# Performance work log

Hardware: AMD Instinct MI355X
Metric: run time of the kernel (lower is better)

The kernel has to match this reference:

```python
import jax, jax.numpy as jnp
import numpy as np

WEIGHT_THRESH = 0.5
EPS = 1e-5
B, N = 4096, 1024


def setup_inputs() -> dict:
    key = jax.random.key(0)
    k1, k2, k3 = jax.random.split(key, 3)
    src = jax.random.normal(k1, (B, N, 3), dtype=jnp.float32)
    tgt = jax.random.normal(k2, (B, N, 3), dtype=jnp.float32)
    w = jax.random.uniform(k3, (B, N), dtype=jnp.float32)
    return {"src_points": src, "tgt_points": tgt, "weights": w}


def _weighted_procrustes(src, ref, w):
    # threshold + normalize weights
    w = jnp.where(w < WEIGHT_THRESH, jnp.zeros_like(w), w)
    w = w / (jnp.sum(w, axis=1, keepdims=True) + EPS)
    w = w[:, :, None]                       # (B, N, 1)
    # weighted centroids
    src_c = jnp.sum(src * w, axis=1, keepdims=True)   # (B, 1, 3)
    ref_c = jnp.sum(ref * w, axis=1, keepdims=True)   # (B, 1, 3)
    src0 = src - src_c
    ref0 = ref - ref_c
    # weighted cross-covariance H = src0^T @ (w * ref0): (B, 3, 3)
    H = jnp.einsum('bni,bnj->bij', src0, w * ref0)
    U, S, Vh = jnp.linalg.svd(H)            # torch.svd returns V, jnp returns Vh
    V = jnp.swapaxes(Vh, 1, 2)
    Ut = jnp.swapaxes(U, 1, 2)
    det = jnp.linalg.det(V @ Ut)            # (B,)
    sgn = jnp.sign(det)
    # D = diag(1, 1, sign(det)); V @ D scales the last column of V
    D = jnp.stack([jnp.ones_like(sgn), jnp.ones_like(sgn), sgn], axis=-1)  # (B, 3)
    R = (V * D[:, None, :]) @ Ut            # (B, 3, 3)
    # t = ref_c - R @ src_c
    t = (jnp.swapaxes(ref_c, 1, 2) - R @ jnp.swapaxes(src_c, 1, 2))[:, :, 0]  # (B, 3)
    return R, t


def reference(src_points, tgt_points, weights):
    return _weighted_procrustes(src_points, tgt_points, weights)
```

## Files before the change

### kernel.cpp

```cpp
#include <hip/hip_runtime.h>
#include <math.h>

#define WTHRESH 0.5f
#define EPSV    1e-5f

__device__ __forceinline__ void gload_lds16(const float4* g, float4* l) {
  __builtin_amdgcn_global_load_lds(
      (const __attribute__((address_space(1))) void*)g,
      (__attribute__((address_space(3))) void*)l, 16, 0, 0);
}

template <int CTRL>
__device__ __forceinline__ float dpp_add(float x) {
  int xi = __builtin_bit_cast(int, x);
  int mv = __builtin_amdgcn_update_dpp(0, xi, CTRL, 0xF, 0xF, true);
  return x + __builtin_bit_cast(float, mv);
}

#define JROT(app,aqq,apq, arp,arq, vAp,vAq, vBp,vBq, vCp,vCq)                 \
  do {                                                                        \
    float _apq = (apq);                                                       \
    if (fabsf(_apq) > 1e-30f) {                                               \
      float _tau = ((aqq) - (app)) * 0.5f / _apq;                             \
      float _t = copysignf(1.0f, _tau) / (fabsf(_tau) + sqrtf(1.0f + _tau*_tau)); \
      float _c = 1.0f / sqrtf(1.0f + _t*_t);                                  \
      float _s = _t * _c;                                                     \
      float _app = (app), _aqq = (aqq);                                       \
      (app) = _app - _t * _apq;                                               \
      (aqq) = _aqq + _t * _apq;                                               \
      (apq) = 0.0f;                                                           \
      float _arp = (arp), _arq = (arq);                                       \
      (arp) = _c * _arp - _s * _arq;                                          \
      (arq) = _s * _arp + _c * _arq;                                          \
      { float _vp=(vAp), _vq=(vAq); (vAp)=_c*_vp-_s*_vq; (vAq)=_s*_vp+_c*_vq; } \
      { float _vp=(vBp), _vq=(vBq); (vBp)=_c*_vp-_s*_vq; (vBq)=_s*_vp+_c*_vq; } \
      { float _vp=(vCp), _vq=(vCq); (vCp)=_c*_vp-_s*_vq; (vCq)=_s*_vp+_c*_vq; } \
    }                                                                         \
  } while (0)

#define CSWAP(li,lj, x0,x1, y0,y1, z0,z1)                                     \
  do { if ((li) < (lj)) {                                                     \
    float _t;                                                                 \
    _t=(li); (li)=(lj); (lj)=_t;                                              \
    _t=(x0); (x0)=(x1); (x1)=_t;                                              \
    _t=(y0); (y0)=(y1); (y1)=_t;                                              \
    _t=(z0); (z0)=(z1); (z1)=_t;                                              \
  } } while (0)

__global__ __launch_bounds__(256) void wproc_reduce(
    const float* __restrict__ src, const float* __restrict__ tgt,
    const float* __restrict__ wts, float* __restrict__ ws)
{
  __shared__ float4 lds[1792];

  const int b    = blockIdx.x;
  const int tid  = threadIdx.x;
  const int wave = tid >> 6;
  const int lane = tid & 63;

  const float4* sg = reinterpret_cast<const float4*>(src + (size_t)b * 3072);
  const float4* tg = reinterpret_cast<const float4*>(tgt + (size_t)b * 3072);
  const float4* wg = reinterpret_cast<const float4*>(wts + (size_t)b * 1024);

  #pragma unroll
  for (int i = 0; i < 3; ++i) {
    const int c = wave * 192 + i * 64;
    gload_lds16(sg + c + lane, &lds[c]);
  }
  #pragma unroll
  for (int i = 0; i < 3; ++i) {
    const int c = wave * 192 + i * 64;
    gload_lds16(tg + c + lane, &lds[768 + c]);
  }
  {
    const int c = wave * 64;
    gload_lds16(wg + c + lane, &lds[1536 + c]);
  }
  __syncthreads();

  float4 sA = lds[3*tid+0], sB = lds[3*tid+1], sC = lds[3*tid+2];
  float4 tA = lds[768 + 3*tid+0], tB = lds[768 + 3*tid+1], tC = lds[768 + 3*tid+2];
  float4 wv = lds[1536 + tid];

  float acc[16];
  #pragma unroll
  for (int k = 0; k < 16; ++k) acc[k] = 0.0f;

  float PX[4][3] = {{sA.x,sA.y,sA.z},{sA.w,sB.x,sB.y},{sB.z,sB.w,sC.x},{sC.y,sC.z,sC.w}};
  float PY[4][3] = {{tA.x,tA.y,tA.z},{tA.w,tB.x,tB.y},{tB.z,tB.w,tC.x},{tC.y,tC.z,tC.w}};
  float WW[4]    = {wv.x, wv.y, wv.z, wv.w};

  #pragma unroll
  for (int k = 0; k < 4; ++k) {
    float w  = (WW[k] < WTHRESH) ? 0.0f : WW[k];
    float x0 = PX[k][0], x1 = PX[k][1], x2 = PX[k][2];
    float y0 = PY[k][0], y1 = PY[k][1], y2 = PY[k][2];
    acc[0] += w;
    acc[1] += w*x0; acc[2] += w*x1; acc[3] += w*x2;
    acc[4] += w*y0; acc[5] += w*y1; acc[6] += w*y2;
    float wx0 = w*x0, wx1 = w*x1, wx2 = w*x2;
    acc[7]  += wx0*y0; acc[8]  += wx0*y1; acc[9]  += wx0*y2;
    acc[10] += wx1*y0; acc[11] += wx1*y1; acc[12] += wx1*y2;
    acc[13] += wx2*y0; acc[14] += wx2*y1; acc[15] += wx2*y2;
  }

  #pragma unroll
  for (int k = 0; k < 16; ++k) acc[k] = dpp_add<0x111>(acc[k]);
  #pragma unroll
  for (int k = 0; k < 16; ++k) acc[k] = dpp_add<0x112>(acc[k]);
  #pragma unroll
  for (int k = 0; k < 16; ++k) acc[k] = dpp_add<0x114>(acc[k]);
  #pragma unroll
  for (int k = 0; k < 16; ++k) acc[k] = dpp_add<0x118>(acc[k]);
  #pragma unroll
  for (int k = 0; k < 16; ++k) acc[k] = dpp_add<0x142>(acc[k]);
  #pragma unroll
  for (int k = 0; k < 16; ++k) acc[k] = dpp_add<0x143>(acc[k]);

  if (lane == 63) {
    float* o = ws + ((size_t)b * 4 + wave) * 16;
    #pragma unroll
    for (int k = 0; k < 16; ++k) o[k] = acc[k];
  }
}

__global__ __launch_bounds__(256) void wproc_svd(
    const float* __restrict__ ws, float* __restrict__ outR,
    float* __restrict__ outT, int B)
{
  const int b = blockIdx.x * 256 + threadIdx.x;
  if (b >= B) return;

  const float4* p4 = reinterpret_cast<const float4*>(ws + (size_t)b * 64);
  float4 F4[4];
  #pragma unroll
  for (int j = 0; j < 4; ++j) {
    float4 a = p4[j], bb = p4[j+4], c = p4[j+8], d = p4[j+12];
    F4[j].x = a.x + bb.x + c.x + d.x;
    F4[j].y = a.y + bb.y + c.y + d.y;
    F4[j].z = a.z + bb.z + c.z + d.z;
    F4[j].w = a.w + bb.w + c.w + d.w;
  }
  float f[16] = {F4[0].x,F4[0].y,F4[0].z,F4[0].w, F4[1].x,F4[1].y,F4[1].z,F4[1].w,
                 F4[2].x,F4[2].y,F4[2].z,F4[2].w, F4[3].x,F4[3].y,F4[3].z,F4[3].w};

  const float inv  = 1.0f / (f[0] + EPSV);
  const float cx0 = f[1]*inv, cx1 = f[2]*inv, cx2 = f[3]*inv;
  const float cy0 = f[4]*inv, cy1 = f[5]*inv, cy2 = f[6]*inv;
  const float ssum = f[0] * inv;
  const float g = 2.0f - ssum;

  float H00 = f[7]*inv  - g*cx0*cy0, H01 = f[8]*inv  - g*cx0*cy1, H02 = f[9]*inv  - g*cx0*cy2;
  float H10 = f[10]*inv - g*cx1*cy0, H11 = f[11]*inv - g*cx1*cy1, H12 = f[12]*inv - g*cx1*cy2;
  float H20 = f[13]*inv - g*cx2*cy0, H21 = f[14]*inv - g*cx2*cy1, H22 = f[15]*inv - g*cx2*cy2;

  float a00 = H00*H00 + H10*H10 + H20*H20;
  float a11 = H01*H01 + H11*H11 + H21*H21;
  float a22 = H02*H02 + H12*H12 + H22*H22;
  float a01 = H00*H01 + H10*H11 + H20*H21;
  float a02 = H00*H02 + H10*H12 + H20*H22;
  float a12 = H01*H02 + H11*H12 + H21*H22;

  float v00=1.f,v01=0.f,v02=0.f, v10=0.f,v11=1.f,v12=0.f, v20=0.f,v21=0.f,v22=1.f;

  #pragma unroll
  for (int sweep = 0; sweep < 8; ++sweep) {
    JROT(a00,a11,a01, a02,a12, v00,v01, v10,v11, v20,v21);
    JROT(a00,a22,a02, a01,a12, v00,v02, v10,v12, v20,v22);
    JROT(a11,a22,a12, a01,a02, v01,v02, v11,v12, v21,v22);
  }

  CSWAP(a00,a11, v00,v01, v10,v11, v20,v21);
  CSWAP(a00,a22, v00,v02, v10,v12, v20,v22);
  CSWAP(a11,a22, v01,v02, v11,v12, v21,v22);

  float u00 = H00*v00 + H01*v10 + H02*v20;
  float u10 = H10*v00 + H11*v10 + H12*v20;
  float u20 = H20*v00 + H21*v10 + H22*v20;
  float u01 = H00*v01 + H01*v11 + H02*v21;
  float u11 = H10*v01 + H11*v11 + H12*v21;
  float u21 = H20*v01 + H21*v11 + H22*v21;
  float u02 = H00*v02 + H01*v12 + H02*v22;
  float u12 = H10*v02 + H11*v12 + H12*v22;
  float u22 = H20*v02 + H21*v12 + H22*v22;

  float n0 = sqrtf(u00*u00 + u10*u10 + u20*u20);
  float n1 = sqrtf(u01*u01 + u11*u11 + u21*u21);
  float n2 = sqrtf(u02*u02 + u12*u12 + u22*u22);

  float R00,R01,R02,R10,R11,R12,R20,R21,R22;

  if (n0 < 1e-20f) {
    R00=1.f;R01=0.f;R02=0.f; R10=0.f;R11=1.f;R12=0.f; R20=0.f;R21=0.f;R22=1.f;
  } else {
    float i0 = 1.0f / n0;
    u00*=i0; u10*=i0; u20*=i0;

    if (n1 > 1e-7f * n0) {
      float i1 = 1.0f / n1;
      u01*=i1; u11*=i1; u21*=i1;
    } else {
      float ax = fabsf(u00), ay = fabsf(u10), az = fabsf(u20);
      float e0,e1,e2;
      if (ax <= ay && ax <= az)      { e0=1.f; e1=0.f; e2=0.f; }
      else if (ay <= az)             { e0=0.f; e1=1.f; e2=0.f; }
      else                           { e0=0.f; e1=0.f; e2=1.f; }
      u01 = u10*e2 - u20*e1;
      u11 = u20*e0 - u00*e2;
      u21 = u00*e1 - u10*e0;
      float nn = 1.0f / sqrtf(u01*u01 + u11*u11 + u21*u21);
      u01*=nn; u11*=nn; u21*=nn;
    }

    if (n2 > 1e-7f * n0) {
      float i2 = 1.0f / n2;
      u02*=i2; u12*=i2; u22*=i2;
    } else {
      u02 = u10*u21 - u20*u11;
      u12 = u20*u01 - u00*u21;
      u22 = u00*u11 - u10*u01;
    }

    float detU = u00*(u11*u22 - u12*u21) - u01*(u10*u22 - u12*u20) + u02*(u10*u21 - u11*u20);
    float detV = v00*(v11*v22 - v12*v21) - v01*(v10*v22 - v12*v20) + v02*(v10*v21 - v11*v20);
    float sgn = (detU * detV < 0.0f) ? -1.0f : 1.0f;

    R00 = v00*u00 + v01*u01 + sgn*v02*u02;
    R01 = v00*u10 + v01*u11 + sgn*v02*u12;
    R02 = v00*u20 + v01*u21 + sgn*v02*u22;
    R10 = v10*u00 + v11*u01 + sgn*v12*u02;
    R11 = v10*u10 + v11*u11 + sgn*v12*u12;
    R12 = v10*u20 + v11*u21 + sgn*v12*u22;
    R20 = v20*u00 + v21*u01 + sgn*v22*u02;
    R21 = v20*u10 + v21*u11 + sgn*v22*u12;
    R22 = v20*u20 + v21*u21 + sgn*v22*u22;
  }

  float t0 = cy0 - (R00*cx0 + R01*cx1 + R02*cx2);
  float t1 = cy1 - (R10*cx0 + R11*cx1 + R12*cx2);
  float t2 = cy2 - (R20*cx0 + R21*cx1 + R22*cx2);

  float* Rb = outR + (size_t)b * 9;
  Rb[0]=R00; Rb[1]=R01; Rb[2]=R02;
  Rb[3]=R10; Rb[4]=R11; Rb[5]=R12;
  Rb[6]=R20; Rb[7]=R21; Rb[8]=R22;
  float* tb = outT + (size_t)b * 3;
  tb[0]=t0; tb[1]=t1; tb[2]=t2;
}

extern "C" void kernel_launch(void* const* d_in, const int* in_sizes, int n_in,
                              void* d_out, int out_size, void* d_ws, size_t ws_size,
                              hipStream_t stream) {
  const float* src = (const float*)d_in[0];
  const float* tgt = (const float*)d_in[1];
  const float* w   = (const float*)d_in[2];

  const int B = in_sizes[2] / 1024;
  float* outR = (float*)d_out;
  float* outT = outR + (size_t)B * 9;
  float* ws   = (float*)d_ws;

  wproc_reduce<<<dim3(B), dim3(256), 0, stream>>>(src, tgt, w, ws);
  wproc_svd<<<dim3((B + 255) / 256), dim3(256), 0, stream>>>(ws, outR, outT, B);
}
```

Measured before the change: 140.9 us.

## Persistent reduce blocks with register double-buffered direct global loads

Replaces the LDS staging via global_load_lds with direct per-thread float4 loads into registers, and makes each block process four batches in a grid-strided loop, prefetching the next batch while reducing the current one. The grid shrinks to B/4 and launch_bounds requests higher occupancy, and the partial-sum stores become float4 writes. The aim is to hide memory latency and cut block launch overhead. In exchange, the per-thread loads are strided (3 float4 per thread), which coalesces less well, and register pressure goes up. It also assumes B is divisible by 4.

```diff
diff --git a/kernel.cpp b/kernel.cpp
--- a/kernel.cpp
+++ b/kernel.cpp
@@ -3,12 +3,6 @@
 
 #define WTHRESH 0.5f
 #define EPSV    1e-5f
-
-__device__ __forceinline__ void gload_lds16(const float4* g, float4* l) {
-  __builtin_amdgcn_global_load_lds(
-      (const __attribute__((address_space(1))) void*)g,
-      (__attribute__((address_space(3))) void*)l, 16, 0, 0);
-}
 
 template <int CTRL>
 __device__ __forceinline__ float dpp_add(float x) {
@@ -47,48 +41,34 @@
     _t=(z0); (z0)=(z1); (z1)=_t;                                              \
   } } while (0)
 
-__global__ __launch_bounds__(256) void wproc_reduce(
-    const float* __restrict__ src, const float* __restrict__ tgt,
-    const float* __restrict__ wts, float* __restrict__ ws)
-{
-  __shared__ float4 lds[1792];
-
-  const int b    = blockIdx.x;
-  const int tid  = threadIdx.x;
-  const int wave = tid >> 6;
-  const int lane = tid & 63;
-
-  const float4* sg = reinterpret_cast<const float4*>(src + (size_t)b * 3072);
-  const float4* tg = reinterpret_cast<const float4*>(tgt + (size_t)b * 3072);
-  const float4* wg = reinterpret_cast<const float4*>(wts + (size_t)b * 1024);
-
-  #pragma unroll
-  for (int i = 0; i < 3; ++i) {
-    const int c = wave * 192 + i * 64;
-    gload_lds16(sg + c + lane, &lds[c]);
-  }
-  #pragma unroll
-  for (int i = 0; i < 3; ++i) {
-    const int c = wave * 192 + i * 64;
-    gload_lds16(tg + c + lane, &lds[768 + c]);
-  }
-  {
-    const int c = wave * 64;
-    gload_lds16(wg + c + lane, &lds[1536 + c]);
-  }
-  __syncthreads();
-
-  float4 sA = lds[3*tid+0], sB = lds[3*tid+1], sC = lds[3*tid+2];
-  float4 tA = lds[768 + 3*tid+0], tB = lds[768 + 3*tid+1], tC = lds[768 + 3*tid+2];
-  float4 wv = lds[1536 + tid];
-
+struct Slice {
+  float4 s0, s1, s2, t0, t1, t2, w;
+};
+
+__device__ __forceinline__ void load_slice(
+    Slice& r, const float* __restrict__ src, const float* __restrict__ tgt,
+    const float* __restrict__ wts, int b, int tid)
+{
+  const float4* s4 = reinterpret_cast<const float4*>(src + (size_t)b * 3072);
+  const float4* t4 = reinterpret_cast<const float4*>(tgt + (size_t)b * 3072);
+  const float4* w4 = reinterpret_cast<const float4*>(wts + (size_t)b * 1024);
+  r.s0 = s4[3*tid+0]; r.s1 = s4[3*tid+1]; r.s2 = s4[3*tid+2];
+  r.t0 = t4[3*tid+0]; r.t1 = t4[3*tid+1]; r.t2 = t4[3*tid+2];
+  r.w  = w4[tid];
+}
+
+__device__ __forceinline__ void process_slice(
+    const Slice& c, float* __restrict__ ws, int b, int wave, int lane)
+{
   float acc[16];
   #pragma unroll
   for (int k = 0; k < 16; ++k) acc[k] = 0.0f;
 
-  float PX[4][3] = {{sA.x,sA.y,sA.z},{sA.w,sB.x,sB.y},{sB.z,sB.w,sC.x},{sC.y,sC.z,sC.w}};
-  float PY[4][3] = {{tA.x,tA.y,tA.z},{tA.w,tB.x,tB.y},{tB.z,tB.w,tC.x},{tC.y,tC.z,tC.w}};
-  float WW[4]    = {wv.x, wv.y, wv.z, wv.w};
+  float PX[4][3] = {{c.s0.x,c.s0.y,c.s0.z},{c.s0.w,c.s1.x,c.s1.y},
+                    {c.s1.z,c.s1.w,c.s2.x},{c.s2.y,c.s2.z,c.s2.w}};
+  float PY[4][3] = {{c.t0.x,c.t0.y,c.t0.z},{c.t0.w,c.t1.x,c.t1.y},
+                    {c.t1.z,c.t1.w,c.t2.x},{c.t2.y,c.t2.z,c.t2.w}};
+  float WW[4]    = {c.w.x, c.w.y, c.w.z, c.w.w};
 
   #pragma unroll
   for (int k = 0; k < 4; ++k) {
@@ -118,9 +98,34 @@
   for (int k = 0; k < 16; ++k) acc[k] = dpp_add<0x143>(acc[k]);
 
   if (lane == 63) {
-    float* o = ws + ((size_t)b * 4 + wave) * 16;
-    #pragma unroll
-    for (int k = 0; k < 16; ++k) o[k] = acc[k];
+    float4* o = reinterpret_cast<float4*>(ws + ((size_t)b * 4 + wave) * 16);
+    o[0] = make_float4(acc[0],  acc[1],  acc[2],  acc[3]);
+    o[1] = make_float4(acc[4],  acc[5],  acc[6],  acc[7]);
+    o[2] = make_float4(acc[8],  acc[9],  acc[10], acc[11]);
+    o[3] = make_float4(acc[12], acc[13], acc[14], acc[15]);
+  }
+}
+
+__global__ __launch_bounds__(256, 4) void wproc_reduce(
+    const float* __restrict__ src, const float* __restrict__ tgt,
+    const float* __restrict__ wts, float* __restrict__ ws)
+{
+  const int tid  = threadIdx.x;
+  const int wave = tid >> 6;
+  const int lane = tid & 63;
+  const int G    = gridDim.x;
+
+  int b = blockIdx.x;
+  Slice cur, nxt;
+  load_slice(cur, src, tgt, wts, b, tid);
+
+  #pragma unroll
+  for (int it = 0; it < 4; ++it) {
+    if (it < 3) load_slice(nxt, src, tgt, wts, b + G, tid);
+    __builtin_amdgcn_sched_barrier(0);
+    process_slice(cur, ws, b, wave, lane);
+    cur = nxt;
+    b += G;
   }
 }
 
@@ -260,6 +265,6 @@
   float* outT = outR + (size_t)B * 9;
   float* ws   = (float*)d_ws;
 
-  wproc_reduce<<<dim3(B), dim3(256), 0, stream>>>(src, tgt, w, ws);
+  wproc_reduce<<<dim3(B / 4), dim3(256), 0, stream>>>(src, tgt, w, ws);
   wproc_svd<<<dim3((B + 255) / 256), dim3(256), 0, stream>>>(ws, outR, outT, B);
 }
```

Result: no change. 142.6 us (+1.2%).

## Make reduce kernel persistent with double-buffered per-wave LDS prefetch

Applied to the files above, without the earlier changes.

Replaces the one-block-per-batch reduce kernel with a persistent grid of 512 blocks. Each block walks several batches and prefetches the next batch into a second LDS buffer through direct global-to-LDS loads, waiting with a partial vmcnt so loads overlap compute. Each wave now owns its own slab, which drops the block-wide __syncthreads, and the partial-sum stores become float4 writes. The risks are a fixed grid of 512, which may underfill the GPU, and the larger LDS footprint of about 57KB, which limits occupancy.

```diff
diff --git a/kernel.cpp b/kernel.cpp
--- a/kernel.cpp
+++ b/kernel.cpp
@@ -47,80 +47,94 @@
     _t=(z0); (z0)=(z1); (z1)=_t;                                              \
   } } while (0)
 
-__global__ __launch_bounds__(256) void wproc_reduce(
+#define SLAB 448
+
+__device__ __forceinline__ void stage_wave(
     const float* __restrict__ src, const float* __restrict__ tgt,
-    const float* __restrict__ wts, float* __restrict__ ws)
+    const float* __restrict__ wts, int b, int wave, int lane, float4* slab)
 {
-  __shared__ float4 lds[1792];
-
-  const int b    = blockIdx.x;
+  const float4* sg = reinterpret_cast<const float4*>(src + (size_t)b * 3072) + wave * 192;
+  const float4* tg = reinterpret_cast<const float4*>(tgt + (size_t)b * 3072) + wave * 192;
+  const float4* wg = reinterpret_cast<const float4*>(wts + (size_t)b * 1024) + wave * 64;
+  #pragma unroll
+  for (int i = 0; i < 3; ++i) gload_lds16(sg + i * 64 + lane, slab + i * 64);
+  #pragma unroll
+  for (int i = 0; i < 3; ++i) gload_lds16(tg + i * 64 + lane, slab + 192 + i * 64);
+  gload_lds16(wg + lane, slab + 384);
+}
+
+__global__ __launch_bounds__(256, 2) void wproc_reduce(
+    const float* __restrict__ src, const float* __restrict__ tgt,
+    const float* __restrict__ wts, float* __restrict__ ws, int NB)
+{
+  __shared__ float4 lds[2][4][SLAB];
+
   const int tid  = threadIdx.x;
   const int wave = tid >> 6;
   const int lane = tid & 63;
-
-  const float4* sg = reinterpret_cast<const float4*>(src + (size_t)b * 3072);
-  const float4* tg = reinterpret_cast<const float4*>(tgt + (size_t)b * 3072);
-  const float4* wg = reinterpret_cast<const float4*>(wts + (size_t)b * 1024);
-
-  #pragma unroll
-  for (int i = 0; i < 3; ++i) {
-    const int c = wave * 192 + i * 64;
-    gload_lds16(sg + c + lane, &lds[c]);
-  }
-  #pragma unroll
-  for (int i = 0; i < 3; ++i) {
-    const int c = wave * 192 + i * 64;
-    gload_lds16(tg + c + lane, &lds[768 + c]);
-  }
-  {
-    const int c = wave * 64;
-    gload_lds16(wg + c + lane, &lds[1536 + c]);
-  }
-  __syncthreads();
-
-  float4 sA = lds[3*tid+0], sB = lds[3*tid+1], sC = lds[3*tid+2];
-  float4 tA = lds[768 + 3*tid+0], tB = lds[768 + 3*tid+1], tC = lds[768 + 3*tid+2];
-  float4 wv = lds[1536 + tid];
-
-  float acc[16];
-  #pragma unroll
-  for (int k = 0; k < 16; ++k) acc[k] = 0.0f;
-
-  float PX[4][3] = {{sA.x,sA.y,sA.z},{sA.w,sB.x,sB.y},{sB.z,sB.w,sC.x},{sC.y,sC.z,sC.w}};
-  float PY[4][3] = {{tA.x,tA.y,tA.z},{tA.w,tB.x,tB.y},{tB.z,tB.w,tC.x},{tC.y,tC.z,tC.w}};
-  float WW[4]    = {wv.x, wv.y, wv.z, wv.w};
-
-  #pragma unroll
-  for (int k = 0; k < 4; ++k) {
-    float w  = (WW[k] < WTHRESH) ? 0.0f : WW[k];
-    float x0 = PX[k][0], x1 = PX[k][1], x2 = PX[k][2];
-    float y0 = PY[k][0], y1 = PY[k][1], y2 = PY[k][2];
-    acc[0] += w;
-    acc[1] += w*x0; acc[2] += w*x1; acc[3] += w*x2;
-    acc[4] += w*y0; acc[5] += w*y1; acc[6] += w*y2;
-    float wx0 = w*x0, wx1 = w*x1, wx2 = w*x2;
-    acc[7]  += wx0*y0; acc[8]  += wx0*y1; acc[9]  += wx0*y2;
-    acc[10] += wx1*y0; acc[11] += wx1*y1; acc[12] += wx1*y2;
-    acc[13] += wx2*y0; acc[14] += wx2*y1; acc[15] += wx2*y2;
-  }
-
-  #pragma unroll
-  for (int k = 0; k < 16; ++k) acc[k] = dpp_add<0x111>(acc[k]);
-  #pragma unroll
-  for (int k = 0; k < 16; ++k) acc[k] = dpp_add<0x112>(acc[k]);
-  #pragma unroll
-  for (int k = 0; k < 16; ++k) acc[k] = dpp_add<0x114>(acc[k]);
-  #pragma unroll
-  for (int k = 0; k < 16; ++k) acc[k] = dpp_add<0x118>(acc[k]);
-  #pragma unroll
-  for (int k = 0; k < 16; ++k) acc[k] = dpp_add<0x142>(acc[k]);
-  #pragma unroll
-  for (int k = 0; k < 16; ++k) acc[k] = dpp_add<0x143>(acc[k]);
-
-  if (lane == 63) {
-    float* o = ws + ((size_t)b * 4 + wave) * 16;
-    #pragma unroll
-    for (int k = 0; k < 16; ++k) o[k] = acc[k];
+  const int G    = gridDim.x;
+
+  int b = blockIdx.x;
+  stage_wave(src, tgt, wts, b, wave, lane, lds[0][wave]);
+
+  for (int it = 0; it < NB; ++it) {
+    const int cur = it & 1;
+    if (it + 1 < NB) {
+      stage_wave(src, tgt, wts, b + G, wave, lane, lds[cur ^ 1][wave]);
+      asm volatile("s_waitcnt vmcnt(7)" ::: "memory");
+    } else {
+      asm volatile("s_waitcnt vmcnt(0)" ::: "memory");
+    }
+    __builtin_amdgcn_sched_barrier(0);
+
+    const float4* slab = lds[cur][wave];
+    float4 sA = slab[3*lane+0], sB = slab[3*lane+1], sC = slab[3*lane+2];
+    float4 tA = slab[192+3*lane+0], tB = slab[192+3*lane+1], tC = slab[192+3*lane+2];
+    float4 wv = slab[384+lane];
+
+    float acc[16];
+    #pragma unroll
+    for (int k = 0; k < 16; ++k) acc[k] = 0.0f;
+
+    float PX[4][3] = {{sA.x,sA.y,sA.z},{sA.w,sB.x,sB.y},{sB.z,sB.w,sC.x},{sC.y,sC.z,sC.w}};
+    float PY[4][3] = {{tA.x,tA.y,tA.z},{tA.w,tB.x,tB.y},{tB.z,tB.w,tC.x},{tC.y,tC.z,tC.w}};
+    float WW[4]    = {wv.x, wv.y, wv.z, wv.w};
+
+    #pragma unroll
+    for (int k = 0; k < 4; ++k) {
+      float w  = (WW[k] < WTHRESH) ? 0.0f : WW[k];
+      float x0 = PX[k][0], x1 = PX[k][1], x2 = PX[k][2];
+      float y0 = PY[k][0], y1 = PY[k][1], y2 = PY[k][2];
+      acc[0] += w;
+      acc[1] += w*x0; acc[2] += w*x1; acc[3] += w*x2;
+      acc[4] += w*y0; acc[5] += w*y1; acc[6] += w*y2;
+      float wx0 = w*x0, wx1 = w*x1, wx2 = w*x2;
+      acc[7]  += wx0*y0; acc[8]  += wx0*y1; acc[9]  += wx0*y2;
+      acc[10] += wx1*y0; acc[11] += wx1*y1; acc[12] += wx1*y2;
+      acc[13] += wx2*y0; acc[14] += wx2*y1; acc[15] += wx2*y2;
+    }
+
+    #pragma unroll
+    for (int k = 0; k < 16; ++k) acc[k] = dpp_add<0x111>(acc[k]);
+    #pragma unroll
+    for (int k = 0; k < 16; ++k) acc[k] = dpp_add<0x112>(acc[k]);
+    #pragma unroll
+    for (int k = 0; k < 16; ++k) acc[k] = dpp_add<0x114>(acc[k]);
+    #pragma unroll
+    for (int k = 0; k < 16; ++k) acc[k] = dpp_add<0x118>(acc[k]);
+    #pragma unroll
+    for (int k = 0; k < 16; ++k) acc[k] = dpp_add<0x142>(acc[k]);
+    #pragma unroll
+    for (int k = 0; k < 16; ++k) acc[k] = dpp_add<0x143>(acc[k]);
+
+    if (lane == 63) {
+      float4* o = reinterpret_cast<float4*>(ws + ((size_t)b * 4 + wave) * 16);
+      o[0] = make_float4(acc[0],  acc[1],  acc[2],  acc[3]);
+      o[1] = make_float4(acc[4],  acc[5],  acc[6],  acc[7]);
+      o[2] = make_float4(acc[8],  acc[9],  acc[10], acc[11]);
+      o[3] = make_float4(acc[12], acc[13], acc[14], acc[15]);
+    }
+    b += G;
   }
 }
 
@@ -260,6 +274,10 @@
   float* outT = outR + (size_t)B * 9;
   float* ws   = (float*)d_ws;
 
-  wproc_reduce<<<dim3(B), dim3(256), 0, stream>>>(src, tgt, w, ws);
+  int grid = 512;
+  if (B % grid != 0) grid = B;
+  const int NB = B / grid;
+
+  wproc_reduce<<<dim3(grid), dim3(256), 0, stream>>>(src, tgt, w, ws, NB);
   wproc_svd<<<dim3((B + 255) / 256), dim3(256), 0, stream>>>(ws, outR, outT, B);
 }
```

After: 141.2 us. About the same (+0.2%).
